# Kernel optimization log

Hardware: AMD Instinct MI355X
Metric: run time of the kernel (lower is better)

The kernel has to match this reference:

```python
import jax, jax.numpy as jnp
import numpy as np
import math

B, C, H, W = 16, 128, 64, 64

def _conv3(x, w, b):
    # 3x3 conv, padding=1 (SAME), NCHW / OIHW
    y = jax.lax.conv_general_dilated(x, w, window_strides=(1, 1), padding='SAME',
                                     dimension_numbers=('NCHW', 'OIHW', 'NCHW'))
    return y + b[None, :, None, None]

def setup_inputs() -> dict:
    key = jax.random.key(0)
    ks = jax.random.split(key, 12)
    s = 0.02
    inp = {
        'F_in': jax.random.normal(ks[0], (B, C, H, W), dtype=jnp.float32),
        'Pspe': jax.random.normal(ks[1], (B, C, C), dtype=jnp.float32),
        'q_w': jax.random.normal(ks[2], (C, C, 3, 3), dtype=jnp.float32) * s,
        'q_b': jnp.zeros((C,), dtype=jnp.float32),
        'k_w': jax.random.normal(ks[3], (C, C, 3, 3), dtype=jnp.float32) * s,
        'k_b': jnp.zeros((C,), dtype=jnp.float32),
        'v_w': jax.random.normal(ks[4], (C, C, 3, 3), dtype=jnp.float32) * s,
        'v_b': jnp.zeros((C,), dtype=jnp.float32),
        'f1_w': jax.random.normal(ks[5], (C, C, 3, 3), dtype=jnp.float32) * s,
        'f1_b': jnp.zeros((C,), dtype=jnp.float32),
        'f2_w': jax.random.normal(ks[6], (C, C, 3, 3), dtype=jnp.float32) * s,
        'f2_b': jnp.zeros((C,), dtype=jnp.float32),
    }
    return inp

def reference(F_in, Pspe, q_w, q_b, k_w, k_b, v_w, v_b, f1_w, f1_b, f2_w, f2_b):
    b, c, h, w = F_in.shape
    hw = h * w
    Qm = _conv3(F_in, q_w, q_b)
    Km = _conv3(F_in, k_w, k_b)
    Vm = _conv3(F_in, v_w, v_b)
    # (B,C,H,W) -> (B,HW,C)
    Q = jnp.transpose(Qm, (0, 2, 3, 1)).reshape(b, hw, c)
    K = jnp.transpose(Km, (0, 2, 3, 1)).reshape(b, hw, c)
    V = jnp.transpose(Vm, (0, 2, 3, 1)).reshape(b, hw, c)
    # channel-wise attention: (B,C,C) = K^T Q, contracting over HW
    attn_logits = jnp.einsum('bnc,bnd->bcd', K, Q) / math.sqrt(hw)
    A = jax.nn.softmax(attn_logits, axis=-1)
    M = jnp.einsum('bce,bed->bcd', Pspe, A)         # prompt fusion
    F3 = jnp.einsum('bnc,bcd->bnd', V, M)           # (B,HW,C)
    F3_map = jnp.transpose(F3.reshape(b, h, w, c), (0, 3, 1, 2))
    # MScanBlock is not defined in the provided source -> identity
    F_ssm = F3_map
    ffn = _conv3(jax.nn.gelu(_conv3(F_ssm, f1_w, f1_b), approximate=False), f2_w, f2_b)
    return F_ssm + ffn
```

## Files before the change

kernel.cpp:

```cpp
#include <hip/hip_runtime.h>
#include <cmath>

typedef unsigned short u16;
typedef __bf16 bf16x8 __attribute__((ext_vector_type(8)));
typedef float f32x4 __attribute__((ext_vector_type(4)));

__device__ __forceinline__ u16 f2bf(float f) {
  unsigned u = __float_as_uint(f);
  u += 0x7fffu + ((u >> 16) & 1u);
  return (u16)(u >> 16);
}
__device__ __forceinline__ float bf2f(u16 h) {
  return __uint_as_float(((unsigned)h) << 16);
}
__device__ __forceinline__ f32x4 mfma_bf16(bf16x8 a, bf16x8 b, f32x4 c) {
  return __builtin_amdgcn_mfma_f32_16x16x32_bf16(a, b, c, 0, 0, 0);
}
__device__ __forceinline__ float gelu_exact(float x) {
  return 0.5f * x * (1.0f + erff(x * 0.70710678118654752440f));
}


__global__ __launch_bounds__(256) void pack_xw(
    const float* __restrict__ Fin, u16* __restrict__ X,
    const float* __restrict__ w0, const float* __restrict__ w1,
    const float* __restrict__ w2, const float* __restrict__ w3,
    const float* __restrict__ w4, u16* __restrict__ Wpk) {
  __shared__ float T[64 * 129];
  const int tid = threadIdx.x;
  if (blockIdx.x < 1024) {
    const int b = blockIdx.x >> 6, y = blockIdx.x & 63;
#pragma unroll
    for (int i = 0; i < 32; ++i) {
      int idx = tid + i * 256;
      int c = idx >> 6, x = idx & 63;
      T[x * 129 + c] = Fin[(size_t)(b * 128 + c) * 4096 + y * 64 + x];
    }
    __syncthreads();
#pragma unroll
    for (int i = 0; i < 4; ++i) {
      int chunk = tid + i * 256;
      int x = chunk >> 4;
      int c0 = (chunk & 15) * 8;
      u16 tmp[8];
#pragma unroll
      for (int e = 0; e < 8; ++e) tmp[e] = f2bf(T[x * 129 + c0 + e]);
      *reinterpret_cast<uint4*>(X + ((size_t)((b * 64 + y) * 64 + x) * 128 + c0)) =
          *reinterpret_cast<const uint4*>(tmp);
    }
  } else {
    int gid = (blockIdx.x - 1024) * 256 + tid;
    int lane = gid & 63;
    int nblk = (gid >> 6) & 7;
    int step = (gid >> 9) % 36;
    int conv = gid / (512 * 36);
    if (conv >= 5) return;
    const float* w = conv == 0 ? w0 : conv == 1 ? w1 : conv == 2 ? w2 : conv == 3 ? w3 : w4;
    int tap = step >> 2, cc = step & 3;
    int dy = tap / 3, dx = tap % 3;
    int co = nblk * 16 + (lane & 15);
    int ci0 = cc * 32 + (lane >> 4) * 8;
    u16 tmp[8];
#pragma unroll
    for (int e = 0; e < 8; ++e)
      tmp[e] = f2bf(w[((size_t)(co * 128 + ci0 + e) * 3 + dy) * 3 + dx]);
    size_t off = ((size_t)conv * 36 * 8 * 64 + (size_t)((step * 8 + nblk) * 64 + lane)) * 8;
    *reinterpret_cast<uint4*>(Wpk + off) = *reinterpret_cast<const uint4*>(tmp);
  }
}

__device__ __forceinline__ void stage_tile(const u16* __restrict__ Xin, u16* Xs,
                                           int tid, int b, int y0) {
#pragma unroll
  for (int i = 0; i < 16; ++i) {
    int j = tid + i * 256;
    int row = j >> 4;
    int c16 = j & 15;
    int ys = row >> 6, x = row & 63;
    int ysrc = y0 - 1 + ys;
    uint4 val = make_uint4(0u, 0u, 0u, 0u);
    if ((unsigned)ysrc < 64u)
      val = *reinterpret_cast<const uint4*>(
          Xin + ((size_t)((b * 64 + ysrc) * 64 + x) * 128 + c16 * 8));
    int xs = x + 1;
    unsigned off = (unsigned)(((ys * 66 + xs) * 128 + c16 * 8) * 2) ^
                   (unsigned)((xs & 7) << 4);
    *reinterpret_cast<uint4*>(reinterpret_cast<char*>(Xs) + off) = val;
  }
  if (tid < 128) {
    int ys = tid >> 5, side = (tid >> 4) & 1, c16 = tid & 15;
    int xs = side ? 65 : 0;
    unsigned off = (unsigned)(((ys * 66 + xs) * 128 + c16 * 8) * 2) ^
                   (unsigned)((xs & 7) << 4);
    *reinterpret_cast<uint4*>(reinterpret_cast<char*>(Xs) + off) =
        make_uint4(0u, 0u, 0u, 0u);
  }
}

__global__ __launch_bounds__(256, 2) void conv_qkv(
    const u16* __restrict__ Xin, const u16* __restrict__ Wp,
    const float* __restrict__ qb, const float* __restrict__ kb,
    const float* __restrict__ vb, u16* __restrict__ QP,
    u16* __restrict__ KP, u16* __restrict__ Vout) {
  __shared__ alignas(16) u16 Xs[4 * 66 * 128];
  const int tid = threadIdx.x;
  const int lane = tid & 63;
  const int wv = tid >> 6;
  const int wm = wv >> 1, wn = wv & 1;
  int mt = blockIdx.x;
  mt = (mt & 7) * 128 + (mt >> 3);
  const int b = mt >> 6;
  const int r = mt & 63;
  const int yp = r >> 1;
  const int nh = r & 1;
  const int y0 = yp * 2;

  stage_tile(Xin, Xs, tid, b, y0);
  __syncthreads();

  f32x4 acc[3][4][2];
#pragma unroll
  for (int c = 0; c < 3; ++c)
#pragma unroll
    for (int i = 0; i < 4; ++i)
#pragma unroll
      for (int j = 0; j < 2; ++j) acc[c][i][j] = f32x4{0.f, 0.f, 0.f, 0.f};

  const int lm = lane & 15, lq = lane >> 4;
  const u16* wb = Wp + (size_t)(((nh * 4 + wn * 2) * 64) + lane) * 8;

  auto loada = [&](bf16x8 (&d)[4], int s) {
    int tap = s >> 2, cc = s & 3;
    int dy = (tap * 11) >> 5;
    int dx = tap - dy * 3;
    int row = (wm + dy) * 66;
#pragma unroll
    for (int i = 0; i < 4; ++i) {
      int xs = i * 16 + lm + dx;
      unsigned off = (unsigned)(((row + xs) * 128 + cc * 32 + lq * 8) * 2) ^
                     (unsigned)((xs & 7) << 4);
      d[i] = *reinterpret_cast<const bf16x8*>(reinterpret_cast<const char*>(Xs) + off);
    }
  };
  auto loadb = [&](bf16x8 (&d)[6], int s) {
#pragma unroll
    for (int cv = 0; cv < 3; ++cv)
#pragma unroll
      for (int j = 0; j < 2; ++j)
        d[cv * 2 + j] = *reinterpret_cast<const bf16x8*>(
            wb + (size_t)cv * 147456 + (size_t)s * 4096 + j * 512);
  };
  auto step = [&](bf16x8 (&a)[4], bf16x8 (&bm)[6]) {
#pragma unroll
    for (int cv = 0; cv < 3; ++cv)
#pragma unroll
      for (int i = 0; i < 4; ++i)
#pragma unroll
        for (int j = 0; j < 2; ++j)
          acc[cv][i][j] = mfma_bf16(a[i], bm[cv * 2 + j], acc[cv][i][j]);
  };

  bf16x8 a0[4], a1[4], b0[6], b1[6];
  loada(a0, 0);
  loadb(b0, 0);
#pragma unroll 1
  for (int s = 0; s < 36; s += 2) {
    loada(a1, s + 1);
    loadb(b1, s + 1);
    step(a0, b0);
    if (s + 2 < 36) {
      loada(a0, s + 2);
      loadb(b0, s + 2);
    }
    step(a1, b1);
  }

  __syncthreads();

  u16* T = Xs;
#pragma unroll
  for (int cv = 0; cv < 2; ++cv) {
    const float* bias = cv == 0 ? qb : kb;
    u16* OutB = cv == 0 ? QP : KP;
#pragma unroll
    for (int i = 0; i < 4; ++i)
#pragma unroll
      for (int j = 0; j < 2; ++j) {
        int nloc = wn * 32 + j * 16 + lm;
        float bs = bias[nh * 64 + nloc];
#pragma unroll
        for (int rr = 0; rr < 4; ++rr) {
          int m = wm * 64 + i * 16 + lq * 4 + rr;
          T[nloc * 136 + m] = f2bf(acc[cv][i][j][rr] + bs);
        }
      }
    __syncthreads();
#pragma unroll
    for (int it = 0; it < 4; ++it) {
      int item = tid + it * 256;
      int l = item & 63, cbl = (item >> 6) & 3, ksl = item >> 8;
      int c = cbl * 16 + (l & 15);
      int mloc = ksl * 32 + (l >> 4) * 8;
      int ks = yp * 4 + ksl, cb = nh * 4 + cbl;
      *reinterpret_cast<uint4*>(
          OutB + (size_t)(((b * 128 + ks) * 8 + cb) * 64 + l) * 8) =
          *reinterpret_cast<const uint4*>(T + c * 136 + mloc);
    }
    __syncthreads();
  }

  u16* Tv = Xs;
#pragma unroll
  for (int i = 0; i < 4; ++i)
#pragma unroll
    for (int j = 0; j < 2; ++j) {
      int nloc = wn * 32 + j * 16 + lm;
      float bs = vb[nh * 64 + nloc];
#pragma unroll
      for (int rr = 0; rr < 4; ++rr) {
        int m = wm * 64 + i * 16 + lq * 4 + rr;
        Tv[m * 72 + nloc] = f2bf(acc[2][i][j][rr] + bs);
      }
    }
  __syncthreads();
  {
    int rr = tid >> 1, q = tid & 1;
    const uint4* src = reinterpret_cast<const uint4*>(Tv + rr * 72 + q * 32);
    uint4* dst = reinterpret_cast<uint4*>(
        Vout + ((size_t)((b * 32 + yp) * 128 + rr) * 128 + nh * 64 + q * 32));
#pragma unroll
    for (int k = 0; k < 4; ++k) dst[k] = src[k];
  }
}

template <int MODE>
__global__ __launch_bounds__(256, 2) void conv_gemm(
    const u16* __restrict__ Xin, const u16* __restrict__ Wp,
    const float* __restrict__ bias, u16* __restrict__ OutB,
    float* __restrict__ OutF, const u16* __restrict__ Fssm) {
  __shared__ alignas(16) u16 Xs[4 * 66 * 128];
  const int tid = threadIdx.x;
  const int lane = tid & 63;
  const int wv = tid >> 6;
  const int wm = wv >> 1, wn = wv & 1;
  int mt = blockIdx.x;
  mt = (mt & 7) * 64 + (mt >> 3);
  const int b = mt >> 5;
  const int y0 = (mt & 31) * 2;

  stage_tile(Xin, Xs, tid, b, y0);
  __syncthreads();

  f32x4 acc[4][4];
#pragma unroll
  for (int i = 0; i < 4; ++i)
#pragma unroll
    for (int j = 0; j < 4; ++j) acc[i][j] = f32x4{0.f, 0.f, 0.f, 0.f};

  const int lm = lane & 15, lq = lane >> 4;
  const u16* wb = Wp + (size_t)((wn * 4 * 64) + lane) * 8;

  auto loada = [&](bf16x8 (&d)[4], int s) {
    int tap = s >> 2, cc = s & 3;
    int dy = (tap * 11) >> 5;
    int dx = tap - dy * 3;
    int row = (wm + dy) * 66;
#pragma unroll
    for (int i = 0; i < 4; ++i) {
      int xs = i * 16 + lm + dx;
      unsigned off = (unsigned)(((row + xs) * 128 + cc * 32 + lq * 8) * 2) ^
                     (unsigned)((xs & 7) << 4);
      d[i] = *reinterpret_cast<const bf16x8*>(reinterpret_cast<const char*>(Xs) + off);
    }
  };
  auto loadb = [&](bf16x8 (&d)[4], int s) {
#pragma unroll
    for (int j = 0; j < 4; ++j)
      d[j] = *reinterpret_cast<const bf16x8*>(wb + (size_t)s * 4096 + j * 512);
  };
  auto step = [&](bf16x8 (&a)[4], bf16x8 (&bm)[4]) {
#pragma unroll
    for (int i = 0; i < 4; ++i)
#pragma unroll
      for (int j = 0; j < 4; ++j) acc[i][j] = mfma_bf16(a[i], bm[j], acc[i][j]);
  };

  bf16x8 a0[4], a1[4], b0[4], b1[4];
  loada(a0, 0);
  loadb(b0, 0);
#pragma unroll 1
  for (int s = 0; s < 36; s += 2) {
    loada(a1, s + 1);
    loadb(b1, s + 1);
    step(a0, b0);
    if (s + 2 < 36) {
      loada(a0, s + 2);
      loadb(b0, s + 2);
    }
    step(a1, b1);
  }

  __syncthreads();

  if (MODE == 1) {
    u16* T = Xs;
#pragma unroll
    for (int i = 0; i < 4; ++i)
#pragma unroll
      for (int j = 0; j < 4; ++j) {
        int n = wn * 64 + j * 16 + lm;
        float bs = bias[n];
#pragma unroll
        for (int r = 0; r < 4; ++r) {
          int m = wm * 64 + i * 16 + lq * 4 + r;
          T[m * 136 + n] = f2bf(gelu_exact(acc[i][j][r] + bs));
        }
      }
    __syncthreads();
    int rr = tid >> 1, hf = tid & 1;
    const uint4* src = reinterpret_cast<const uint4*>(T + rr * 136 + hf * 64);
    uint4* dst = reinterpret_cast<uint4*>(OutB + ((size_t)(mt * 128 + rr) * 128 + hf * 64));
#pragma unroll
    for (int k = 0; k < 8; ++k) dst[k] = src[k];
  } else {
    float* T = reinterpret_cast<float*>(Xs);
#pragma unroll
    for (int i = 0; i < 4; ++i)
#pragma unroll
      for (int j = 0; j < 4; ++j) {
        int n = wn * 64 + j * 16 + lm;
        float bs = bias[n];
#pragma unroll
        for (int r = 0; r < 4; ++r) {
          int m = wm * 64 + i * 16 + lq * 4 + r;
          float v = acc[i][j][r] + bs + bf2f(Fssm[(size_t)(mt * 128 + m) * 128 + n]);
          T[n * 132 + m] = v;
        }
      }
    __syncthreads();
    int rr = tid >> 1, hf = tid & 1;
    const uint4* src = reinterpret_cast<const uint4*>(T + rr * 132 + hf * 64);
    uint4* dst = reinterpret_cast<uint4*>(
        OutF + ((size_t)(b * 128 + rr) * 4096 + (mt & 31) * 128 + hf * 64));
#pragma unroll
    for (int k = 0; k < 16; ++k) dst[k] = src[k];
  }
}

__global__ __launch_bounds__(256, 2) void attn_s(const u16* __restrict__ QP,
                                                 const u16* __restrict__ KP,
                                                 float* __restrict__ SP) {
  const int tid = threadIdx.x;
  const int lane = tid & 63;
  const int wv = tid >> 6, wm = wv >> 1, wn = wv & 1;
  const int lm = lane & 15, lq = lane >> 4;
  int mt = blockIdx.x;
  mt = (mt & 7) * 16 + (mt >> 3);
  const int b = mt >> 3, sp = mt & 7;

  f32x4 acc[4][4];
#pragma unroll
  for (int i = 0; i < 4; ++i)
#pragma unroll
    for (int j = 0; j < 4; ++j) acc[i][j] = f32x4{0.f, 0.f, 0.f, 0.f};

#pragma unroll
  for (int ksl = 0; ksl < 16; ++ksl) {
    const int ks = sp * 16 + ksl;
    bf16x8 af[4], bfr[4];
#pragma unroll
    for (int i = 0; i < 4; ++i)
      af[i] = *reinterpret_cast<const bf16x8*>(
          KP + (size_t)(((b * 128 + ks) * 8 + wm * 4 + i) * 64 + lane) * 8);
#pragma unroll
    for (int j = 0; j < 4; ++j)
      bfr[j] = *reinterpret_cast<const bf16x8*>(
          QP + (size_t)(((b * 128 + ks) * 8 + wn * 4 + j) * 64 + lane) * 8);
#pragma unroll
    for (int i = 0; i < 4; ++i)
#pragma unroll
      for (int j = 0; j < 4; ++j) acc[i][j] = mfma_bf16(af[i], bfr[j], acc[i][j]);
  }

  float* out = SP + (size_t)(b * 8 + sp) * 16384;
#pragma unroll
  for (int i = 0; i < 4; ++i)
#pragma unroll
    for (int j = 0; j < 4; ++j)
#pragma unroll
      for (int r = 0; r < 4; ++r)
        out[(wm * 64 + i * 16 + lq * 4 + r) * 128 + wn * 64 + j * 16 + lm] =
            acc[i][j][r];
}

__global__ __launch_bounds__(256) void attn_r(const float* __restrict__ SP,
                                              u16* __restrict__ ABP) {
  __shared__ float Sf[32][129];
  __shared__ float Inv[32];
  const int tid = threadIdx.x;
  const int b = blockIdx.x >> 2, eb = blockIdx.x & 3;

#pragma unroll
  for (int it = 0; it < 16; ++it) {
    int id = it * 256 + tid;
    int rl = id >> 7, d = id & 127;
    const float* p = SP + (size_t)b * 8 * 16384 + (size_t)(eb * 32 + rl) * 128 + d;
    float s = 0.f;
#pragma unroll
    for (int sp = 0; sp < 8; ++sp) s += p[(size_t)sp * 16384];
    Sf[rl][d] = s * 0.015625f;
  }
  __syncthreads();

  {
    int rl = tid >> 3, sub = tid & 7;
    float mx = -3.4e38f;
#pragma unroll
    for (int k = 0; k < 16; ++k) mx = fmaxf(mx, Sf[rl][sub + 8 * k]);
    mx = fmaxf(mx, __shfl_xor(mx, 1));
    mx = fmaxf(mx, __shfl_xor(mx, 2));
    mx = fmaxf(mx, __shfl_xor(mx, 4));
    float s = 0.f;
#pragma unroll
    for (int k = 0; k < 16; ++k) {
      float e = __expf(Sf[rl][sub + 8 * k] - mx);
      Sf[rl][sub + 8 * k] = e;
      s += e;
    }
    s += __shfl_xor(s, 1);
    s += __shfl_xor(s, 2);
    s += __shfl_xor(s, 4);
    if (sub == 0) Inv[rl] = 1.0f / s;
  }
  __syncthreads();

#pragma unroll
  for (int it = 0; it < 2; ++it) {
    int item = tid + it * 256;
    int l = item & 63, nb = item >> 6;
    int d = nb * 16 + (l & 15);
    u16 tmp[8];
#pragma unroll
    for (int e = 0; e < 8; ++e) {
      int rloc = (l >> 4) * 8 + e;
      tmp[e] = f2bf(Sf[rloc][d] * Inv[rloc]);
    }
    *reinterpret_cast<uint4*>(ABP + (size_t)(((b * 4 + eb) * 8 + nb) * 64 + l) * 8) =
        *reinterpret_cast<const uint4*>(tmp);
  }
}

__global__ __launch_bounds__(256, 1) void attn_m(const float* __restrict__ Pspe,
                                                 const u16* __restrict__ ABP,
                                                 u16* __restrict__ Mpack) {
  __shared__ u16 Ml[128 * 136];
  const int b = blockIdx.x;
  const int tid = threadIdx.x;
  const int lane = tid & 63;
  const int wv = tid >> 6, wm = wv >> 1, wn = wv & 1;
  const int lm = lane & 15, lq = lane >> 4;

  f32x4 acc[4][4];
#pragma unroll
  for (int i = 0; i < 4; ++i)
#pragma unroll
    for (int j = 0; j < 4; ++j) acc[i][j] = f32x4{0.f, 0.f, 0.f, 0.f};

  const float* P = Pspe + (size_t)b * 128 * 128;
#pragma unroll
  for (int cc = 0; cc < 4; ++cc) {
    int e0 = cc * 32 + lq * 8;
    bf16x8 af[4], bfr[4];
#pragma unroll
    for (int i = 0; i < 4; ++i) {
      const float* p = P + (size_t)(wm * 64 + i * 16 + lm) * 128 + e0;
      union { u16 u[8]; bf16x8 v; } cv;
#pragma unroll
      for (int e = 0; e < 8; ++e) cv.u[e] = f2bf(p[e]);
      af[i] = cv.v;
    }
#pragma unroll
    for (int j = 0; j < 4; ++j)
      bfr[j] = *reinterpret_cast<const bf16x8*>(
          ABP + (size_t)(((b * 4 + cc) * 8 + wn * 4 + j) * 64 + lane) * 8);
#pragma unroll
    for (int i = 0; i < 4; ++i)
#pragma unroll
      for (int j = 0; j < 4; ++j) acc[i][j] = mfma_bf16(af[i], bfr[j], acc[i][j]);
  }

#pragma unroll
  for (int i = 0; i < 4; ++i)
#pragma unroll
    for (int j = 0; j < 4; ++j)
#pragma unroll
      for (int r = 0; r < 4; ++r)
        Ml[(wn * 64 + j * 16 + lm) * 136 + (wm * 64 + i * 16 + lq * 4 + r)] =
            f2bf(acc[i][j][r]);
  __syncthreads();

#pragma unroll
  for (int it = 0; it < 8; ++it) {
    int item = tid + it * 256;
    int l2 = item & 63, nb = (item >> 6) & 7, cc2 = item >> 9;
    int d = nb * 16 + (l2 & 15), c0 = cc2 * 32 + (l2 >> 4) * 8;
    *reinterpret_cast<uint4*>(Mpack + (size_t)b * 16384 + (size_t)item * 8) =
        *reinterpret_cast<const uint4*>(Ml + d * 136 + c0);
  }
}

__global__ __launch_bounds__(256) void f3_gemm(const u16* __restrict__ V,
                                               const u16* __restrict__ Mpack,
                                               u16* __restrict__ Fout) {
  const int tid = threadIdx.x;
  const int lane = tid & 63;
  const int wv = tid >> 6, wm = wv >> 1, wn = wv & 1;
  const int lm = lane & 15, lq = lane >> 4;
  int mt = blockIdx.x;
  mt = (mt & 7) * 64 + (mt >> 3);
  const int b = mt >> 5;

  f32x4 acc[4][4];
#pragma unroll
  for (int i = 0; i < 4; ++i)
#pragma unroll
    for (int j = 0; j < 4; ++j) acc[i][j] = f32x4{0.f, 0.f, 0.f, 0.f};

#pragma unroll
  for (int cc = 0; cc < 4; ++cc) {
    int k0 = cc * 32 + lq * 8;
    bf16x8 af[4], bfr[4];
#pragma unroll
    for (int i = 0; i < 4; ++i)
      af[i] = *reinterpret_cast<const bf16x8*>(
          V + (size_t)(mt * 128 + wm * 64 + i * 16 + lm) * 128 + k0);
#pragma unroll
    for (int j = 0; j < 4; ++j)
      bfr[j] = *reinterpret_cast<const bf16x8*>(
          Mpack + (size_t)b * 16384 + (size_t)((cc * 8 + wn * 4 + j) * 64 + lane) * 8);
#pragma unroll
    for (int i = 0; i < 4; ++i)
#pragma unroll
      for (int j = 0; j < 4; ++j) acc[i][j] = mfma_bf16(af[i], bfr[j], acc[i][j]);
  }

  __shared__ u16 T[128 * 136];
#pragma unroll
  for (int i = 0; i < 4; ++i)
#pragma unroll
    for (int j = 0; j < 4; ++j)
#pragma unroll
      for (int r = 0; r < 4; ++r)
        T[(wm * 64 + i * 16 + lq * 4 + r) * 136 + wn * 64 + j * 16 + lm] =
            f2bf(acc[i][j][r]);
  __syncthreads();
  int rr = tid >> 1, hf = tid & 1;
  const uint4* src = reinterpret_cast<const uint4*>(T + rr * 136 + hf * 64);
  uint4* dst = reinterpret_cast<uint4*>(Fout + ((size_t)(mt * 128 + rr) * 128 + hf * 64));
#pragma unroll
  for (int k = 0; k < 8; ++k) dst[k] = src[k];
}

extern "C" void kernel_launch(void* const* d_in, const int* in_sizes, int n_in,
                              void* d_out, int out_size, void* d_ws, size_t ws_size,
                              hipStream_t stream) {
  const float* F_in = (const float*)d_in[0];
  const float* Pspe = (const float*)d_in[1];
  const float* q_w = (const float*)d_in[2];
  const float* q_b = (const float*)d_in[3];
  const float* k_w = (const float*)d_in[4];
  const float* k_b = (const float*)d_in[5];
  const float* v_w = (const float*)d_in[6];
  const float* v_b = (const float*)d_in[7];
  const float* f1_w = (const float*)d_in[8];
  const float* f1_b = (const float*)d_in[9];
  const float* f2_w = (const float*)d_in[10];
  const float* f2_b = (const float*)d_in[11];
  float* out = (float*)d_out;

  char* ws = (char*)d_ws;
  const size_t SZ = 16777216;
  u16* X = (u16*)(ws);
  u16* QP = (u16*)(ws + SZ);
  u16* KP = (u16*)(ws + 2 * SZ);
  u16* V = (u16*)(ws + 3 * SZ);
  u16* Wpk = (u16*)(ws + 4 * SZ);
  u16* Mpk = (u16*)(ws + 4 * SZ + 1474560);
  float* SP = (float*)ws;
  u16* ABP = KP;
  u16* Fssm = X;
  u16* Hid = QP;

  pack_xw<<<1384, 256, 0, stream>>>(F_in, X, q_w, k_w, v_w, f1_w, f2_w, Wpk);
  conv_qkv<<<1024, 256, 0, stream>>>(X, Wpk, q_b, k_b, v_b, QP, KP, V);
  attn_s<<<128, 256, 0, stream>>>(QP, KP, SP);
  attn_r<<<64, 256, 0, stream>>>(SP, ABP);
  attn_m<<<16, 256, 0, stream>>>(Pspe, ABP, Mpk);
  f3_gemm<<<512, 256, 0, stream>>>(V, Mpk, Fssm);
  conv_gemm<1><<<512, 256, 0, stream>>>(Fssm, Wpk + 3 * 147456, f1_b, Hid, nullptr, nullptr);
  conv_gemm<3><<<512, 256, 0, stream>>>(Hid, Wpk + 4 * 147456, f2_b, nullptr, out, Fssm);
}
```

Baseline: 176.9 us.

## Use zero-padded activation buffers and read conv operands directly from global memory

Activations now live in zero-padded (66x66) NHWC buffers, with the borders zeroed in spare blocks of pack_xw and f3_gemm. This lets the conv kernels drop the shared-memory tile staging and load MFMA A fragments straight from global memory at tap offsets. Shared memory use falls, so the occupancy hints rise to 3 and 4 blocks per SM, and the final conv writes float4 outputs directly without an LDS transpose. The trade-off is that the main loop is no longer software-pipelined and relies on cache hits for the nine-fold reuse of each input element across taps. The risk is global-load latency that the LDS tile used to hide.

```diff
diff --git a/kernel.cpp b/kernel.cpp
--- a/kernel.cpp
+++ b/kernel.cpp
@@ -20,16 +20,27 @@
   return 0.5f * x * (1.0f + erff(x * 0.70710678118654752440f));
 }
 
+__device__ __forceinline__ size_t pidx(int b, int y, int x) {
+  return ((size_t)(b * 66 + y) * 66 + x) * 128;
+}
+
+__device__ __forceinline__ void border_yx(int k, int& y, int& x) {
+  if (k < 66) { y = 0; x = k; }
+  else if (k < 132) { y = 65; x = k - 66; }
+  else if (k < 196) { y = k - 131; x = 0; }
+  else { y = k - 195; x = 65; }
+}
 
 __global__ __launch_bounds__(256) void pack_xw(
-    const float* __restrict__ Fin, u16* __restrict__ X,
+    const float* __restrict__ Fin, u16* __restrict__ Xp,
     const float* __restrict__ w0, const float* __restrict__ w1,
     const float* __restrict__ w2, const float* __restrict__ w3,
     const float* __restrict__ w4, u16* __restrict__ Wpk) {
-  __shared__ float T[64 * 129];
-  const int tid = threadIdx.x;
-  if (blockIdx.x < 1024) {
-    const int b = blockIdx.x >> 6, y = blockIdx.x & 63;
+  const int tid = threadIdx.x;
+  const int bid = blockIdx.x;
+  if (bid < 1024) {
+    __shared__ float T[64 * 129];
+    const int b = bid >> 6, y = bid & 63;
 #pragma unroll
     for (int i = 0; i < 32; ++i) {
       int idx = tid + i * 256;
@@ -45,11 +56,11 @@
       u16 tmp[8];
 #pragma unroll
       for (int e = 0; e < 8; ++e) tmp[e] = f2bf(T[x * 129 + c0 + e]);
-      *reinterpret_cast<uint4*>(X + ((size_t)((b * 64 + y) * 64 + x) * 128 + c0)) =
+      *reinterpret_cast<uint4*>(Xp + pidx(b, y + 1, x + 1) + c0) =
           *reinterpret_cast<const uint4*>(tmp);
     }
-  } else {
-    int gid = (blockIdx.x - 1024) * 256 + tid;
+  } else if (bid < 1384) {
+    int gid = (bid - 1024) * 256 + tid;
     int lane = gid & 63;
     int nblk = (gid >> 6) & 7;
     int step = (gid >> 9) % 36;
@@ -66,43 +77,22 @@
       tmp[e] = f2bf(w[((size_t)(co * 128 + ci0 + e) * 3 + dy) * 3 + dx]);
     size_t off = ((size_t)conv * 36 * 8 * 64 + (size_t)((step * 8 + nblk) * 64 + lane)) * 8;
     *reinterpret_cast<uint4*>(Wpk + off) = *reinterpret_cast<const uint4*>(tmp);
-  }
-}
-
-__device__ __forceinline__ void stage_tile(const u16* __restrict__ Xin, u16* Xs,
-                                           int tid, int b, int y0) {
-#pragma unroll
-  for (int i = 0; i < 16; ++i) {
-    int j = tid + i * 256;
-    int row = j >> 4;
-    int c16 = j & 15;
-    int ys = row >> 6, x = row & 63;
-    int ysrc = y0 - 1 + ys;
-    uint4 val = make_uint4(0u, 0u, 0u, 0u);
-    if ((unsigned)ysrc < 64u)
-      val = *reinterpret_cast<const uint4*>(
-          Xin + ((size_t)((b * 64 + ysrc) * 64 + x) * 128 + c16 * 8));
-    int xs = x + 1;
-    unsigned off = (unsigned)(((ys * 66 + xs) * 128 + c16 * 8) * 2) ^
-                   (unsigned)((xs & 7) << 4);
-    *reinterpret_cast<uint4*>(reinterpret_cast<char*>(Xs) + off) = val;
-  }
-  if (tid < 128) {
-    int ys = tid >> 5, side = (tid >> 4) & 1, c16 = tid & 15;
-    int xs = side ? 65 : 0;
-    unsigned off = (unsigned)(((ys * 66 + xs) * 128 + c16 * 8) * 2) ^
-                   (unsigned)((xs & 7) << 4);
-    *reinterpret_cast<uint4*>(reinterpret_cast<char*>(Xs) + off) =
+  } else {
+    int p = (bid - 1384) * 16 + (tid >> 4);
+    int b = p / 260, k = p % 260;
+    int y, x;
+    border_yx(k, y, x);
+    *reinterpret_cast<uint4*>(Xp + pidx(b, y, x) + (tid & 15) * 8) =
         make_uint4(0u, 0u, 0u, 0u);
   }
 }
 
-__global__ __launch_bounds__(256, 2) void conv_qkv(
-    const u16* __restrict__ Xin, const u16* __restrict__ Wp,
+__global__ __launch_bounds__(256, 3) void conv_qkv(
+    const u16* __restrict__ Xp, const u16* __restrict__ Wp,
     const float* __restrict__ qb, const float* __restrict__ kb,
     const float* __restrict__ vb, u16* __restrict__ QP,
     u16* __restrict__ KP, u16* __restrict__ Vout) {
-  __shared__ alignas(16) u16 Xs[4 * 66 * 128];
+  __shared__ alignas(16) u16 Ts[128 * 72];
   const int tid = threadIdx.x;
   const int lane = tid & 63;
   const int wv = tid >> 6;
@@ -114,9 +104,17 @@
   const int yp = r >> 1;
   const int nh = r & 1;
   const int y0 = yp * 2;
-
-  stage_tile(Xin, Xs, tid, b, y0);
-  __syncthreads();
+  const int lm = lane & 15, lq = lane >> 4;
+
+  const char* ab[4];
+#pragma unroll
+  for (int i = 0; i < 4; ++i) {
+    int pos = wm * 64 + i * 16 + lm;
+    int y = y0 + (pos >> 6), x = pos & 63;
+    ab[i] = reinterpret_cast<const char*>(Xp + pidx(b, y, x) + lq * 8);
+  }
+  const char* wb = reinterpret_cast<const char*>(
+      Wp + (size_t)(((nh * 4 + wn * 2) * 64) + lane) * 8);
 
   f32x4 acc[3][4][2];
 #pragma unroll
@@ -126,58 +124,31 @@
 #pragma unroll
       for (int j = 0; j < 2; ++j) acc[c][i][j] = f32x4{0.f, 0.f, 0.f, 0.f};
 
-  const int lm = lane & 15, lq = lane >> 4;
-  const u16* wb = Wp + (size_t)(((nh * 4 + wn * 2) * 64) + lane) * 8;
-
-  auto loada = [&](bf16x8 (&d)[4], int s) {
-    int tap = s >> 2, cc = s & 3;
-    int dy = (tap * 11) >> 5;
-    int dx = tap - dy * 3;
-    int row = (wm + dy) * 66;
-#pragma unroll
-    for (int i = 0; i < 4; ++i) {
-      int xs = i * 16 + lm + dx;
-      unsigned off = (unsigned)(((row + xs) * 128 + cc * 32 + lq * 8) * 2) ^
-                     (unsigned)((xs & 7) << 4);
-      d[i] = *reinterpret_cast<const bf16x8*>(reinterpret_cast<const char*>(Xs) + off);
-    }
-  };
-  auto loadb = [&](bf16x8 (&d)[6], int s) {
+#pragma unroll 1
+  for (int s = 0; s < 36; ++s) {
+    const int tap = s >> 2, cc = s & 3;
+    const int dy = (tap * 11) >> 5;
+    const int dx = tap - dy * 3;
+    const int aoff = dy * 16896 + dx * 256 + cc * 64;
+    bf16x8 af[4], bfr[6];
+#pragma unroll
+    for (int i = 0; i < 4; ++i)
+      af[i] = *reinterpret_cast<const bf16x8*>(ab[i] + aoff);
 #pragma unroll
     for (int cv = 0; cv < 3; ++cv)
 #pragma unroll
       for (int j = 0; j < 2; ++j)
-        d[cv * 2 + j] = *reinterpret_cast<const bf16x8*>(
-            wb + (size_t)cv * 147456 + (size_t)s * 4096 + j * 512);
-  };
-  auto step = [&](bf16x8 (&a)[4], bf16x8 (&bm)[6]) {
+        bfr[cv * 2 + j] = *reinterpret_cast<const bf16x8*>(
+            wb + cv * 294912 + s * 8192 + j * 1024);
 #pragma unroll
     for (int cv = 0; cv < 3; ++cv)
 #pragma unroll
       for (int i = 0; i < 4; ++i)
 #pragma unroll
         for (int j = 0; j < 2; ++j)
-          acc[cv][i][j] = mfma_bf16(a[i], bm[cv * 2 + j], acc[cv][i][j]);
-  };
-
-  bf16x8 a0[4], a1[4], b0[6], b1[6];
-  loada(a0, 0);
-  loadb(b0, 0);
-#pragma unroll 1
-  for (int s = 0; s < 36; s += 2) {
-    loada(a1, s + 1);
-    loadb(b1, s + 1);
-    step(a0, b0);
-    if (s + 2 < 36) {
-      loada(a0, s + 2);
-      loadb(b0, s + 2);
-    }
-    step(a1, b1);
-  }
-
-  __syncthreads();
-
-  u16* T = Xs;
+          acc[cv][i][j] = mfma_bf16(af[i], bfr[cv * 2 + j], acc[cv][i][j]);
+  }
+
 #pragma unroll
   for (int cv = 0; cv < 2; ++cv) {
     const float* bias = cv == 0 ? qb : kb;
@@ -191,7 +162,7 @@
 #pragma unroll
         for (int rr = 0; rr < 4; ++rr) {
           int m = wm * 64 + i * 16 + lq * 4 + rr;
-          T[nloc * 136 + m] = f2bf(acc[cv][i][j][rr] + bs);
+          Ts[nloc * 136 + m] = f2bf(acc[cv][i][j][rr] + bs);
         }
       }
     __syncthreads();
@@ -204,12 +175,11 @@
       int ks = yp * 4 + ksl, cb = nh * 4 + cbl;
       *reinterpret_cast<uint4*>(
           OutB + (size_t)(((b * 128 + ks) * 8 + cb) * 64 + l) * 8) =
-          *reinterpret_cast<const uint4*>(T + c * 136 + mloc);
+          *reinterpret_cast<const uint4*>(Ts + c * 136 + mloc);
     }
     __syncthreads();
   }
 
-  u16* Tv = Xs;
 #pragma unroll
   for (int i = 0; i < 4; ++i)
 #pragma unroll
@@ -219,13 +189,13 @@
 #pragma unroll
       for (int rr = 0; rr < 4; ++rr) {
         int m = wm * 64 + i * 16 + lq * 4 + rr;
-        Tv[m * 72 + nloc] = f2bf(acc[2][i][j][rr] + bs);
+        Ts[m * 72 + nloc] = f2bf(acc[2][i][j][rr] + bs);
       }
     }
   __syncthreads();
   {
     int rr = tid >> 1, q = tid & 1;
-    const uint4* src = reinterpret_cast<const uint4*>(Tv + rr * 72 + q * 32);
+    const uint4* src = reinterpret_cast<const uint4*>(Ts + rr * 72 + q * 32);
     uint4* dst = reinterpret_cast<uint4*>(
         Vout + ((size_t)((b * 32 + yp) * 128 + rr) * 128 + nh * 64 + q * 32));
 #pragma unroll
@@ -234,11 +204,10 @@
 }
 
 template <int MODE>
-__global__ __launch_bounds__(256, 2) void conv_gemm(
+__global__ __launch_bounds__(256, 4) void conv_ffn(
     const u16* __restrict__ Xin, const u16* __restrict__ Wp,
-    const float* __restrict__ bias, u16* __restrict__ OutB,
-    float* __restrict__ OutF, const u16* __restrict__ Fssm) {
-  __shared__ alignas(16) u16 Xs[4 * 66 * 128];
+    const float* __restrict__ bias, u16* __restrict__ OutP,
+    float* __restrict__ OutF, const u16* __restrict__ Resid) {
   const int tid = threadIdx.x;
   const int lane = tid & 63;
   const int wv = tid >> 6;
@@ -246,10 +215,19 @@
   int mt = blockIdx.x;
   mt = (mt & 7) * 64 + (mt >> 3);
   const int b = mt >> 5;
-  const int y0 = (mt & 31) * 2;
-
-  stage_tile(Xin, Xs, tid, b, y0);
-  __syncthreads();
+  const int yp = mt & 31;
+  const int y0 = yp * 2;
+  const int lm = lane & 15, lq = lane >> 4;
+
+  const char* ab[4];
+#pragma unroll
+  for (int i = 0; i < 4; ++i) {
+    int pos = wm * 64 + i * 16 + lm;
+    int y = y0 + (pos >> 6), x = pos & 63;
+    ab[i] = reinterpret_cast<const char*>(Xin + pidx(b, y, x) + lq * 8);
+  }
+  const char* wb = reinterpret_cast<const char*>(
+      Wp + (size_t)((wn * 4 * 64) + lane) * 8);
 
   f32x4 acc[4][4];
 #pragma unroll
@@ -257,53 +235,27 @@
 #pragma unroll
     for (int j = 0; j < 4; ++j) acc[i][j] = f32x4{0.f, 0.f, 0.f, 0.f};
 
-  const int lm = lane & 15, lq = lane >> 4;
-  const u16* wb = Wp + (size_t)((wn * 4 * 64) + lane) * 8;
-
-  auto loada = [&](bf16x8 (&d)[4], int s) {
-    int tap = s >> 2, cc = s & 3;
-    int dy = (tap * 11) >> 5;
-    int dx = tap - dy * 3;
-    int row = (wm + dy) * 66;
-#pragma unroll
-    for (int i = 0; i < 4; ++i) {
-      int xs = i * 16 + lm + dx;
-      unsigned off = (unsigned)(((row + xs) * 128 + cc * 32 + lq * 8) * 2) ^
-                     (unsigned)((xs & 7) << 4);
-      d[i] = *reinterpret_cast<const bf16x8*>(reinterpret_cast<const char*>(Xs) + off);
-    }
-  };
-  auto loadb = [&](bf16x8 (&d)[4], int s) {
-#pragma unroll
-    for (int j = 0; j < 4; ++j)
-      d[j] = *reinterpret_cast<const bf16x8*>(wb + (size_t)s * 4096 + j * 512);
-  };
-  auto step = [&](bf16x8 (&a)[4], bf16x8 (&bm)[4]) {
-#pragma unroll
-    for (int i = 0; i < 4; ++i)
-#pragma unroll
-      for (int j = 0; j < 4; ++j) acc[i][j] = mfma_bf16(a[i], bm[j], acc[i][j]);
-  };
-
-  bf16x8 a0[4], a1[4], b0[4], b1[4];
-  loada(a0, 0);
-  loadb(b0, 0);
 #pragma unroll 1
-  for (int s = 0; s < 36; s += 2) {
-    loada(a1, s + 1);
-    loadb(b1, s + 1);
-    step(a0, b0);
-    if (s + 2 < 36) {
-      loada(a0, s + 2);
-      loadb(b0, s + 2);
-    }
-    step(a1, b1);
-  }
-
-  __syncthreads();
-
-  if (MODE == 1) {
-    u16* T = Xs;
+  for (int s = 0; s < 36; ++s) {
+    const int tap = s >> 2, cc = s & 3;
+    const int dy = (tap * 11) >> 5;
+    const int dx = tap - dy * 3;
+    const int aoff = dy * 16896 + dx * 256 + cc * 64;
+    bf16x8 af[4], bfr[4];
+#pragma unroll
+    for (int i = 0; i < 4; ++i)
+      af[i] = *reinterpret_cast<const bf16x8*>(ab[i] + aoff);
+#pragma unroll
+    for (int j = 0; j < 4; ++j)
+      bfr[j] = *reinterpret_cast<const bf16x8*>(wb + s * 8192 + j * 1024);
+#pragma unroll
+    for (int i = 0; i < 4; ++i)
+#pragma unroll
+      for (int j = 0; j < 4; ++j) acc[i][j] = mfma_bf16(af[i], bfr[j], acc[i][j]);
+  }
+
+  if constexpr (MODE == 1) {
+    __shared__ u16 T[128 * 136];
 #pragma unroll
     for (int i = 0; i < 4; ++i)
 #pragma unroll
@@ -318,32 +270,29 @@
       }
     __syncthreads();
     int rr = tid >> 1, hf = tid & 1;
+    int y = y0 + (rr >> 6), x = rr & 63;
     const uint4* src = reinterpret_cast<const uint4*>(T + rr * 136 + hf * 64);
-    uint4* dst = reinterpret_cast<uint4*>(OutB + ((size_t)(mt * 128 + rr) * 128 + hf * 64));
+    uint4* dst = reinterpret_cast<uint4*>(OutP + pidx(b, y + 1, x + 1) + hf * 64);
 #pragma unroll
     for (int k = 0; k < 8; ++k) dst[k] = src[k];
   } else {
-    float* T = reinterpret_cast<float*>(Xs);
 #pragma unroll
     for (int i = 0; i < 4; ++i)
 #pragma unroll
       for (int j = 0; j < 4; ++j) {
         int n = wn * 64 + j * 16 + lm;
         float bs = bias[n];
-#pragma unroll
-        for (int r = 0; r < 4; ++r) {
-          int m = wm * 64 + i * 16 + lq * 4 + r;
-          float v = acc[i][j][r] + bs + bf2f(Fssm[(size_t)(mt * 128 + m) * 128 + n]);
-          T[n * 132 + m] = v;
-        }
+        int m0 = wm * 64 + i * 16 + lq * 4;
+        int y = y0 + (m0 >> 6), x = m0 & 63;
+        const u16* rp = Resid + pidx(b, y + 1, x + 1) + n;
+        float4 v;
+        v.x = acc[i][j][0] + bs + bf2f(rp[0]);
+        v.y = acc[i][j][1] + bs + bf2f(rp[128]);
+        v.z = acc[i][j][2] + bs + bf2f(rp[256]);
+        v.w = acc[i][j][3] + bs + bf2f(rp[384]);
+        *reinterpret_cast<float4*>(
+            OutF + ((size_t)(b * 128 + n) * 4096 + yp * 128 + m0)) = v;
       }
-    __syncthreads();
-    int rr = tid >> 1, hf = tid & 1;
-    const uint4* src = reinterpret_cast<const uint4*>(T + rr * 132 + hf * 64);
-    uint4* dst = reinterpret_cast<uint4*>(
-        OutF + ((size_t)(b * 128 + rr) * 4096 + (mt & 31) * 128 + hf * 64));
-#pragma unroll
-    for (int k = 0; k < 16; ++k) dst[k] = src[k];
   }
 }
 
@@ -511,14 +460,17 @@
 
 __global__ __launch_bounds__(256) void f3_gemm(const u16* __restrict__ V,
                                                const u16* __restrict__ Mpack,
-                                               u16* __restrict__ Fout) {
+                                               u16* __restrict__ Fp,
+                                               u16* __restrict__ Hp) {
   const int tid = threadIdx.x;
   const int lane = tid & 63;
   const int wv = tid >> 6, wm = wv >> 1, wn = wv & 1;
   const int lm = lane & 15, lq = lane >> 4;
-  int mt = blockIdx.x;
+  const int bid = blockIdx.x;
+  int mt = bid;
   mt = (mt & 7) * 64 + (mt >> 3);
   const int b = mt >> 5;
+  const int yp = mt & 31;
 
   f32x4 acc[4][4];
 #pragma unroll
@@ -542,6 +494,20 @@
     for (int i = 0; i < 4; ++i)
 #pragma unroll
       for (int j = 0; j < 4; ++j) acc[i][j] = mfma_bf16(af[i], bfr[j], acc[i][j]);
+  }
+
+#pragma unroll
+  for (int rep = 0; rep < 2; ++rep) {
+    int p = bid * 32 + rep * 16 + (tid >> 4);
+    if (p < 8320) {
+      u16* buf = p < 4160 ? Fp : Hp;
+      int q = p < 4160 ? p : p - 4160;
+      int bb = q / 260, k = q % 260;
+      int y, x;
+      border_yx(k, y, x);
+      *reinterpret_cast<uint4*>(buf + pidx(bb, y, x) + (tid & 15) * 8) =
+          make_uint4(0u, 0u, 0u, 0u);
+    }
   }
 
   __shared__ u16 T[128 * 136];
@@ -555,8 +521,9 @@
             f2bf(acc[i][j][r]);
   __syncthreads();
   int rr = tid >> 1, hf = tid & 1;
+  int y = yp * 2 + (rr >> 6), x = rr & 63;
   const uint4* src = reinterpret_cast<const uint4*>(T + rr * 136 + hf * 64);
-  uint4* dst = reinterpret_cast<uint4*>(Fout + ((size_t)(mt * 128 + rr) * 128 + hf * 64));
+  uint4* dst = reinterpret_cast<uint4*>(Fp + pidx(b, y + 1, x + 1) + hf * 64);
 #pragma unroll
   for (int k = 0; k < 8; ++k) dst[k] = src[k];
 }
@@ -579,24 +546,29 @@
   float* out = (float*)d_out;
 
   char* ws = (char*)d_ws;
-  const size_t SZ = 16777216;
-  u16* X = (u16*)(ws);
-  u16* QP = (u16*)(ws + SZ);
-  u16* KP = (u16*)(ws + 2 * SZ);
-  u16* V = (u16*)(ws + 3 * SZ);
-  u16* Wpk = (u16*)(ws + 4 * SZ);
-  u16* Mpk = (u16*)(ws + 4 * SZ + 1474560);
-  float* SP = (float*)ws;
+  const size_t XPO = 0;
+  const size_t QPO = 17842176;
+  const size_t KPO = QPO + 16777216;
+  const size_t VO  = KPO + 16777216;
+  const size_t WPO = VO + 16777216;
+
+  u16* Xp = (u16*)(ws + XPO);
+  u16* QP = (u16*)(ws + QPO);
+  u16* KP = (u16*)(ws + KPO);
+  u16* V = (u16*)(ws + VO);
+  u16* Wpk = (u16*)(ws + WPO);
+  float* SP = (float*)(ws + XPO);
   u16* ABP = KP;
-  u16* Fssm = X;
-  u16* Hid = QP;
-
-  pack_xw<<<1384, 256, 0, stream>>>(F_in, X, q_w, k_w, v_w, f1_w, f2_w, Wpk);
-  conv_qkv<<<1024, 256, 0, stream>>>(X, Wpk, q_b, k_b, v_b, QP, KP, V);
+  u16* Mpk = (u16*)(ws + KPO + 1179648);
+  u16* Fp = Xp;
+  u16* Hp = QP;
+
+  pack_xw<<<1644, 256, 0, stream>>>(F_in, Xp, q_w, k_w, v_w, f1_w, f2_w, Wpk);
+  conv_qkv<<<1024, 256, 0, stream>>>(Xp, Wpk, q_b, k_b, v_b, QP, KP, V);
   attn_s<<<128, 256, 0, stream>>>(QP, KP, SP);
   attn_r<<<64, 256, 0, stream>>>(SP, ABP);
   attn_m<<<16, 256, 0, stream>>>(Pspe, ABP, Mpk);
-  f3_gemm<<<512, 256, 0, stream>>>(V, Mpk, Fssm);
-  conv_gemm<1><<<512, 256, 0, stream>>>(Fssm, Wpk + 3 * 147456, f1_b, Hid, nullptr, nullptr);
-  conv_gemm<3><<<512, 256, 0, stream>>>(Hid, Wpk + 4 * 147456, f2_b, nullptr, out, Fssm);
-}
+  f3_gemm<<<512, 256, 0, stream>>>(V, Mpk, Fp, Hp);
+  conv_ffn<1><<<512, 256, 0, stream>>>(Fp, Wpk + 3 * 147456, f1_b, Hp, nullptr, nullptr);
+  conv_ffn<2><<<512, 256, 0, stream>>>(Hp, Wpk + 4 * 147456, f2_b, nullptr, out, Fp);
+}
```

Result: slower. 278.4 us (+57.4%).

## Fold attention matrix into conv1 weights and recompute residual in conv2 epilogue

Applied to the files above, without the earlier changes.

Instead of materializing F3 = V·M, the per-batch M is folded into the f1 conv weights (per-batch weight set computed by a new wfold1 kernel), so conv1 reads V directly. The residual F3 is recomputed inside the final conv epilogue from V and M with a small MFMA GEMM rather than re-read from memory. attn_r and attn_m are merged into one per-batch kernel that also emits a transposed M pack. This removes the f3_gemm launch and its intermediate round trip, but conv1 now loads batch-specific weights and the extra bf16 rounding of the folded weights may shift numerics.

```diff
diff --git a/kernel.cpp b/kernel.cpp
--- a/kernel.cpp
+++ b/kernel.cpp
@@ -237,7 +237,8 @@
 __global__ __launch_bounds__(256, 2) void conv_gemm(
     const u16* __restrict__ Xin, const u16* __restrict__ Wp,
     const float* __restrict__ bias, u16* __restrict__ OutB,
-    float* __restrict__ OutF, const u16* __restrict__ Fssm) {
+    float* __restrict__ OutF, const u16* __restrict__ Vin,
+    const u16* __restrict__ Mpk) {
   __shared__ alignas(16) u16 Xs[4 * 66 * 128];
   const int tid = threadIdx.x;
   const int lane = tid & 63;
@@ -258,7 +259,8 @@
     for (int j = 0; j < 4; ++j) acc[i][j] = f32x4{0.f, 0.f, 0.f, 0.f};
 
   const int lm = lane & 15, lq = lane >> 4;
-  const u16* wb = Wp + (size_t)((wn * 4 * 64) + lane) * 8;
+  const u16* wb = Wp + (MODE == 1 ? (size_t)b * 147456 : (size_t)0) +
+                  (size_t)((wn * 4 * 64) + lane) * 8;
 
   auto loada = [&](bf16x8 (&d)[4], int s) {
     int tap = s >> 2, cc = s & 3;
@@ -323,6 +325,29 @@
 #pragma unroll
     for (int k = 0; k < 8; ++k) dst[k] = src[k];
   } else {
+    f32x4 accR[4][4];
+#pragma unroll
+    for (int i = 0; i < 4; ++i)
+#pragma unroll
+      for (int j = 0; j < 4; ++j) accR[i][j] = f32x4{0.f, 0.f, 0.f, 0.f};
+#pragma unroll
+    for (int cc = 0; cc < 4; ++cc) {
+      int k0 = cc * 32 + lq * 8;
+      bf16x8 af[4], bfr[4];
+#pragma unroll
+      for (int i = 0; i < 4; ++i)
+        af[i] = *reinterpret_cast<const bf16x8*>(
+            Vin + (size_t)(mt * 128 + wm * 64 + i * 16 + lm) * 128 + k0);
+#pragma unroll
+      for (int j = 0; j < 4; ++j)
+        bfr[j] = *reinterpret_cast<const bf16x8*>(
+            Mpk + (size_t)b * 16384 + (size_t)((cc * 8 + wn * 4 + j) * 64 + lane) * 8);
+#pragma unroll
+      for (int i = 0; i < 4; ++i)
+#pragma unroll
+        for (int j = 0; j < 4; ++j) accR[i][j] = mfma_bf16(af[i], bfr[j], accR[i][j]);
+    }
+
     float* T = reinterpret_cast<float*>(Xs);
 #pragma unroll
     for (int i = 0; i < 4; ++i)
@@ -333,8 +358,7 @@
 #pragma unroll
         for (int r = 0; r < 4; ++r) {
           int m = wm * 64 + i * 16 + lq * 4 + r;
-          float v = acc[i][j][r] + bs + bf2f(Fssm[(size_t)(mt * 128 + m) * 128 + n]);
-          T[n * 132 + m] = v;
+          T[n * 132 + m] = acc[i][j][r] + bs + accR[i][j][r];
         }
       }
     __syncthreads();
@@ -393,79 +417,56 @@
             acc[i][j][r];
 }
 
-__global__ __launch_bounds__(256) void attn_r(const float* __restrict__ SP,
-                                              u16* __restrict__ ABP) {
-  __shared__ float Sf[32][129];
-  __shared__ float Inv[32];
-  const int tid = threadIdx.x;
-  const int b = blockIdx.x >> 2, eb = blockIdx.x & 3;
-
-#pragma unroll
-  for (int it = 0; it < 16; ++it) {
-    int id = it * 256 + tid;
-    int rl = id >> 7, d = id & 127;
-    const float* p = SP + (size_t)b * 8 * 16384 + (size_t)(eb * 32 + rl) * 128 + d;
-    float s = 0.f;
-#pragma unroll
-    for (int sp = 0; sp < 8; ++sp) s += p[(size_t)sp * 16384];
-    Sf[rl][d] = s * 0.015625f;
-  }
-  __syncthreads();
-
-  {
-    int rl = tid >> 3, sub = tid & 7;
-    float mx = -3.4e38f;
-#pragma unroll
-    for (int k = 0; k < 16; ++k) mx = fmaxf(mx, Sf[rl][sub + 8 * k]);
-    mx = fmaxf(mx, __shfl_xor(mx, 1));
-    mx = fmaxf(mx, __shfl_xor(mx, 2));
-    mx = fmaxf(mx, __shfl_xor(mx, 4));
-    float s = 0.f;
-#pragma unroll
-    for (int k = 0; k < 16; ++k) {
-      float e = __expf(Sf[rl][sub + 8 * k] - mx);
-      Sf[rl][sub + 8 * k] = e;
-      s += e;
-    }
-    s += __shfl_xor(s, 1);
-    s += __shfl_xor(s, 2);
-    s += __shfl_xor(s, 4);
-    if (sub == 0) Inv[rl] = 1.0f / s;
-  }
-  __syncthreads();
-
-#pragma unroll
-  for (int it = 0; it < 2; ++it) {
-    int item = tid + it * 256;
-    int l = item & 63, nb = item >> 6;
-    int d = nb * 16 + (l & 15);
-    u16 tmp[8];
-#pragma unroll
-    for (int e = 0; e < 8; ++e) {
-      int rloc = (l >> 4) * 8 + e;
-      tmp[e] = f2bf(Sf[rloc][d] * Inv[rloc]);
-    }
-    *reinterpret_cast<uint4*>(ABP + (size_t)(((b * 4 + eb) * 8 + nb) * 64 + l) * 8) =
-        *reinterpret_cast<const uint4*>(tmp);
-  }
-}
-
-__global__ __launch_bounds__(256, 1) void attn_m(const float* __restrict__ Pspe,
-                                                 const u16* __restrict__ ABP,
-                                                 u16* __restrict__ Mpack) {
-  __shared__ u16 Ml[128 * 136];
+__global__ __launch_bounds__(256, 1) void attn_rm(const float* __restrict__ SP,
+                                                  const float* __restrict__ Pspe,
+                                                  u16* __restrict__ Mpack,
+                                                  u16* __restrict__ Mpack2) {
+  __shared__ float Sf[128 * 129];
+  __shared__ u16 AT[128 * 136];
   const int b = blockIdx.x;
   const int tid = threadIdx.x;
   const int lane = tid & 63;
   const int wv = tid >> 6, wm = wv >> 1, wn = wv & 1;
   const int lm = lane & 15, lq = lane >> 4;
 
-  f32x4 acc[4][4];
-#pragma unroll
-  for (int i = 0; i < 4; ++i)
-#pragma unroll
-    for (int j = 0; j < 4; ++j) acc[i][j] = f32x4{0.f, 0.f, 0.f, 0.f};
-
+#pragma unroll
+  for (int it = 0; it < 64; ++it) {
+    int id = it * 256 + tid;
+    int rl = id >> 7, d = id & 127;
+    const float* p = SP + (size_t)b * 8 * 16384 + (size_t)rl * 128 + d;
+    float s = 0.f;
+#pragma unroll
+    for (int sp = 0; sp < 8; ++sp) s += p[(size_t)sp * 16384];
+    Sf[rl * 129 + d] = s * 0.015625f;
+  }
+  __syncthreads();
+
+  {
+    int c = tid >> 1, hf = tid & 1;
+    float* row = Sf + c * 129 + hf * 64;
+    float mx = -3.4e38f;
+#pragma unroll
+    for (int k = 0; k < 64; ++k) mx = fmaxf(mx, row[k]);
+    mx = fmaxf(mx, __shfl_xor(mx, 1));
+    float s = 0.f;
+#pragma unroll
+    for (int k = 0; k < 64; ++k) {
+      float e = __expf(row[k] - mx);
+      row[k] = e;
+      s += e;
+    }
+    s += __shfl_xor(s, 1);
+    float inv = 1.0f / s;
+#pragma unroll
+    for (int k = 0; k < 64; ++k) AT[(hf * 64 + k) * 136 + c] = f2bf(row[k] * inv);
+  }
+  __syncthreads();
+
+  f32x4 acc2[4][4];
+#pragma unroll
+  for (int i = 0; i < 4; ++i)
+#pragma unroll
+    for (int j = 0; j < 4; ++j) acc2[i][j] = f32x4{0.f, 0.f, 0.f, 0.f};
   const float* P = Pspe + (size_t)b * 128 * 128;
 #pragma unroll
   for (int cc = 0; cc < 4; ++cc) {
@@ -474,21 +475,21 @@
 #pragma unroll
     for (int i = 0; i < 4; ++i) {
       const float* p = P + (size_t)(wm * 64 + i * 16 + lm) * 128 + e0;
-      union { u16 u[8]; bf16x8 v; } cv;
-#pragma unroll
-      for (int e = 0; e < 8; ++e) cv.u[e] = f2bf(p[e]);
-      af[i] = cv.v;
+      union { u16 u[8]; bf16x8 v; } cvt;
+#pragma unroll
+      for (int e = 0; e < 8; ++e) cvt.u[e] = f2bf(p[e]);
+      af[i] = cvt.v;
     }
 #pragma unroll
     for (int j = 0; j < 4; ++j)
-      bfr[j] = *reinterpret_cast<const bf16x8*>(
-          ABP + (size_t)(((b * 4 + cc) * 8 + wn * 4 + j) * 64 + lane) * 8);
-#pragma unroll
-    for (int i = 0; i < 4; ++i)
-#pragma unroll
-      for (int j = 0; j < 4; ++j) acc[i][j] = mfma_bf16(af[i], bfr[j], acc[i][j]);
-  }
-
+      bfr[j] = *reinterpret_cast<const bf16x8*>(AT + (wn * 64 + j * 16 + lm) * 136 + e0);
+#pragma unroll
+    for (int i = 0; i < 4; ++i)
+#pragma unroll
+      for (int j = 0; j < 4; ++j) acc2[i][j] = mfma_bf16(af[i], bfr[j], acc2[i][j]);
+  }
+
+  u16* Ml = reinterpret_cast<u16*>(Sf);
 #pragma unroll
   for (int i = 0; i < 4; ++i)
 #pragma unroll
@@ -496,7 +497,7 @@
 #pragma unroll
       for (int r = 0; r < 4; ++r)
         Ml[(wn * 64 + j * 16 + lm) * 136 + (wm * 64 + i * 16 + lq * 4 + r)] =
-            f2bf(acc[i][j][r]);
+            f2bf(acc2[i][j][r]);
   __syncthreads();
 
 #pragma unroll
@@ -507,18 +508,28 @@
     *reinterpret_cast<uint4*>(Mpack + (size_t)b * 16384 + (size_t)item * 8) =
         *reinterpret_cast<const uint4*>(Ml + d * 136 + c0);
   }
-}
-
-__global__ __launch_bounds__(256) void f3_gemm(const u16* __restrict__ V,
-                                               const u16* __restrict__ Mpack,
-                                               u16* __restrict__ Fout) {
+#pragma unroll
+  for (int it = 0; it < 8; ++it) {
+    int item = tid + it * 256;
+    int l2 = item & 63, nb = (item >> 6) & 7, cc2 = item >> 9;
+    int c = nb * 16 + (l2 & 15), d0 = cc2 * 32 + (l2 >> 4) * 8;
+    u16 tmp[8];
+#pragma unroll
+    for (int e = 0; e < 8; ++e) tmp[e] = Ml[(d0 + e) * 136 + c];
+    *reinterpret_cast<uint4*>(Mpack2 + (size_t)b * 16384 + (size_t)item * 8) =
+        *reinterpret_cast<const uint4*>(tmp);
+  }
+}
+
+__global__ __launch_bounds__(256, 2) void wfold1(const u16* __restrict__ W1pk,
+                                                 const u16* __restrict__ Mpk2,
+                                                 u16* __restrict__ Wf1) {
+  __shared__ u16 T[128 * 136];
   const int tid = threadIdx.x;
-  const int lane = tid & 63;
-  const int wv = tid >> 6, wm = wv >> 1, wn = wv & 1;
+  const int lane = tid & 63, wv = tid >> 6;
+  const int wm = wv >> 1, wn = wv & 1;
   const int lm = lane & 15, lq = lane >> 4;
-  int mt = blockIdx.x;
-  mt = (mt & 7) * 64 + (mt >> 3);
-  const int b = mt >> 5;
+  const int b = blockIdx.x / 9, tap = blockIdx.x % 9;
 
   f32x4 acc[4][4];
 #pragma unroll
@@ -528,23 +539,21 @@
 
 #pragma unroll
   for (int cc = 0; cc < 4; ++cc) {
-    int k0 = cc * 32 + lq * 8;
     bf16x8 af[4], bfr[4];
 #pragma unroll
     for (int i = 0; i < 4; ++i)
       af[i] = *reinterpret_cast<const bf16x8*>(
-          V + (size_t)(mt * 128 + wm * 64 + i * 16 + lm) * 128 + k0);
+          W1pk + (size_t)(((tap * 4 + cc) * 8 + wm * 4 + i) * 64 + lane) * 8);
 #pragma unroll
     for (int j = 0; j < 4; ++j)
       bfr[j] = *reinterpret_cast<const bf16x8*>(
-          Mpack + (size_t)b * 16384 + (size_t)((cc * 8 + wn * 4 + j) * 64 + lane) * 8);
+          Mpk2 + (size_t)b * 16384 + (size_t)((cc * 8 + wn * 4 + j) * 64 + lane) * 8);
 #pragma unroll
     for (int i = 0; i < 4; ++i)
 #pragma unroll
       for (int j = 0; j < 4; ++j) acc[i][j] = mfma_bf16(af[i], bfr[j], acc[i][j]);
   }
 
-  __shared__ u16 T[128 * 136];
 #pragma unroll
   for (int i = 0; i < 4; ++i)
 #pragma unroll
@@ -554,11 +563,18 @@
         T[(wm * 64 + i * 16 + lq * 4 + r) * 136 + wn * 64 + j * 16 + lm] =
             f2bf(acc[i][j][r]);
   __syncthreads();
-  int rr = tid >> 1, hf = tid & 1;
-  const uint4* src = reinterpret_cast<const uint4*>(T + rr * 136 + hf * 64);
-  uint4* dst = reinterpret_cast<uint4*>(Fout + ((size_t)(mt * 128 + rr) * 128 + hf * 64));
-#pragma unroll
-  for (int k = 0; k < 8; ++k) dst[k] = src[k];
+
+#pragma unroll
+  for (int it = 0; it < 8; ++it) {
+    int item = tid + it * 256;
+    int L = item & 63, nb = (item >> 6) & 7, cc2 = item >> 9;
+    int co = nb * 16 + (L & 15);
+    int c0 = cc2 * 32 + (L >> 4) * 8;
+    *reinterpret_cast<uint4*>(
+        Wf1 + (size_t)b * 147456 +
+        ((size_t)(((tap * 4 + cc2) * 8 + nb) * 64 + L)) * 8) =
+        *reinterpret_cast<const uint4*>(T + co * 136 + c0);
+  }
 }
 
 extern "C" void kernel_launch(void* const* d_in, const int* in_sizes, int n_in,
@@ -586,17 +602,18 @@
   u16* V = (u16*)(ws + 3 * SZ);
   u16* Wpk = (u16*)(ws + 4 * SZ);
   u16* Mpk = (u16*)(ws + 4 * SZ + 1474560);
+  u16* Mpk2 = (u16*)(ws + 4 * SZ + 1998848);
+  u16* Wf1 = (u16*)(ws + 4 * SZ + 2523136);
   float* SP = (float*)ws;
-  u16* ABP = KP;
-  u16* Fssm = X;
   u16* Hid = QP;
 
   pack_xw<<<1384, 256, 0, stream>>>(F_in, X, q_w, k_w, v_w, f1_w, f2_w, Wpk);
   conv_qkv<<<1024, 256, 0, stream>>>(X, Wpk, q_b, k_b, v_b, QP, KP, V);
   attn_s<<<128, 256, 0, stream>>>(QP, KP, SP);
-  attn_r<<<64, 256, 0, stream>>>(SP, ABP);
-  attn_m<<<16, 256, 0, stream>>>(Pspe, ABP, Mpk);
-  f3_gemm<<<512, 256, 0, stream>>>(V, Mpk, Fssm);
-  conv_gemm<1><<<512, 256, 0, stream>>>(Fssm, Wpk + 3 * 147456, f1_b, Hid, nullptr, nullptr);
-  conv_gemm<3><<<512, 256, 0, stream>>>(Hid, Wpk + 4 * 147456, f2_b, nullptr, out, Fssm);
-}
+  attn_rm<<<16, 256, 0, stream>>>(SP, Pspe, Mpk, Mpk2);
+  wfold1<<<144, 256, 0, stream>>>(Wpk + 3 * 147456, Mpk2, Wf1);
+  conv_gemm<1><<<512, 256, 0, stream>>>(V, Wf1, f1_b, Hid, nullptr, nullptr,
+                                        nullptr);
+  conv_gemm<3><<<512, 256, 0, stream>>>(Hid, Wpk + 4 * 147456, f2_b, nullptr,
+                                        out, V, Mpk);
+}
```

After: 177.6 us. No clear change (+0.4%).
